# Performance work log

Measured on AMD Instinct MI355X. Metric: run time of the kernel, lower is better.

The kernel has to match this reference:

```python
import jax, jax.numpy as jnp
import numpy as np

NODELEN = 17949
N_NODES = 512
N_EDGES = 4096
H2 = 768
EMB = 128
IN_DIM = 2 * NODELEN


def _seg_mean(h, src, dst, n):
    # gather neighbor features and mean-reduce per destination node
    msg = h[src]                                   # [E, F]
    s = jax.ops.segment_sum(msg, dst, num_segments=n)
    deg = jax.ops.segment_sum(jnp.ones((src.shape[0],), h.dtype), dst, num_segments=n)
    return s / jnp.maximum(deg, 1.0)[:, None]


def setup_inputs() -> dict:
    key = jax.random.key(0)
    ks = jax.random.split(key, 12)
    s = 0.02
    return {
        "x": jax.random.normal(ks[0], (N_NODES, NODELEN), jnp.float32),
        "edge_src": jax.random.randint(ks[1], (N_EDGES,), 0, N_NODES),
        "edge_dst": jax.random.randint(ks[2], (N_EDGES,), 0, N_NODES),
        "W_e2": jax.random.normal(ks[3], (H2, IN_DIM), jnp.float32) * s,
        "b_e2": jnp.zeros((H2,), jnp.float32),
        "W_e3": jax.random.normal(ks[4], (EMB, H2), jnp.float32) * s,
        "b_e3": jnp.zeros((EMB,), jnp.float32),
        "W_d1": jax.random.normal(ks[5], (H2, EMB), jnp.float32) * s,
        "b_d1": jnp.zeros((H2,), jnp.float32),
        "W_d3": jax.random.normal(ks[6], (IN_DIM, H2), jnp.float32) * s,
        "b_d3": jnp.zeros((IN_DIM,), jnp.float32),
    }


def reference(x, edge_src, edge_dst, W_e2, b_e2, W_e3, b_e3, W_d1, b_d1, W_d3, b_d3):
    n = x.shape[0]
    # depth-2 recursive GraphSAGE mean aggregation; agg[0]=0 after each hop
    h1 = _seg_mean(x, edge_src, edge_dst, n).at[:, 0].set(0.0)
    h2 = _seg_mean(h1, edge_src, edge_dst, n).at[:, 0].set(0.0)
    emb = jnp.concatenate([x, h2], axis=1)           # [N, 2*NODELEN]
    emb = emb.at[:, 0].set(0.0).at[:, NODELEN].set(0.0)
    # AutoEncoder (eval mode: dropout is identity)
    h = jax.nn.relu(emb @ W_e2.T + b_e2)
    encoded = h @ W_e3.T + b_e3
    h = jax.nn.relu(encoded @ W_d1.T + b_d1)
    decoded = h @ W_d3.T + b_d3
    return encoded, decoded
```

## Files before the change

### kernel.cpp

```cpp
#include <hip/hip_runtime.h>
#include <hip/hip_bf16.h>

#define NODELEN 17949
#define NN 512
#define NE 4096
#define H2 768
#define EMB 128
#define IN_DIM (2 * NODELEN)
#define KP1 35904
#define KITERS1 561
#define SPLITS 24
#define KCHUNK1 24

#define BM 128
#define BN 128
#define BK 64
#define LDT (BK + 8)

typedef __bf16 bf16x8 __attribute__((ext_vector_type(8)));
typedef float f32x4 __attribute__((ext_vector_type(4)));


__global__ void k_zero_int(int* p, int n) {
    int i = blockIdx.x * 256 + threadIdx.x;
    if (i < n) p[i] = 0;
}

__global__ void k_zero_f4(float4* p, int n4) {
    int i = blockIdx.x * 256 + threadIdx.x;
    if (i < n4) p[i] = make_float4(0.f, 0.f, 0.f, 0.f);
}

__global__ void k_deg(const int* __restrict__ dst, int* __restrict__ cnt) {
    int e = blockIdx.x * 256 + threadIdx.x;
    if (e < NE) atomicAdd(&cnt[dst[e]], 1);
}

__global__ void k_invdeg(const int* __restrict__ cnt, float* __restrict__ invdeg) {
    int i = blockIdx.x * 256 + threadIdx.x;
    if (i < NN) {
        int c = cnt[i];
        invdeg[i] = 1.0f / (float)(c > 1 ? c : 1);
    }
}

__global__ void k_scatter(const int* __restrict__ src, const int* __restrict__ dst,
                          const float* __restrict__ invdeg, float* __restrict__ A) {
    int e = blockIdx.x * 256 + threadIdx.x;
    if (e < NE) {
        int d = dst[e];
        atomicAdd(&A[(size_t)d * NN + src[e]], invdeg[d]);
    }
}

__global__ void k_a2(const float* __restrict__ A, __bf16* __restrict__ A2b) {
    int i = blockIdx.x;
    int t = threadIdx.x;
    __shared__ float row[NN];
    row[t] = A[(size_t)i * NN + t];
    row[t + 256] = A[(size_t)i * NN + 256 + t];
    __syncthreads();
    float a0 = 0.f, a1 = 0.f;
    for (int s = 0; s < NN; ++s) {
        float a = row[s];
        if (a != 0.f) {
            a0 += a * A[(size_t)s * NN + t];
            a1 += a * A[(size_t)s * NN + 256 + t];
        }
    }
    A2b[(size_t)i * NN + t] = (__bf16)a0;
    A2b[(size_t)i * NN + 256 + t] = (__bf16)a1;
}

__global__ void k_xt(const float* __restrict__ x, __bf16* __restrict__ xT) {
    __shared__ float t[64][65];
    int f0 = blockIdx.x * 64, s0 = blockIdx.y * 64;
    int tx = threadIdx.x & 63, ty = threadIdx.x >> 6;
#pragma unroll
    for (int r = 0; r < 16; ++r) {
        int f = f0 + tx;
        t[ty * 16 + r][tx] = (f < NODELEN) ? x[(size_t)(s0 + ty * 16 + r) * NODELEN + f] : 0.f;
    }
    __syncthreads();
#pragma unroll
    for (int r = 0; r < 16; ++r) {
        int f = f0 + ty * 16 + r;
        if (f < NODELEN) xT[(size_t)f * NN + s0 + tx] = (__bf16)t[tx][ty * 16 + r];
    }
}

__global__ void k_embx(const float* __restrict__ x, __bf16* __restrict__ embb) {
    int c = blockIdx.x * 256 + threadIdx.x;
    int n = blockIdx.y;
    if (c < NODELEN) {
        float v = (c == 0) ? 0.f : x[(size_t)n * NODELEN + c];
        embb[(size_t)n * KP1 + c] = (__bf16)v;
    } else {
        int cc = c - NODELEN;
        if (cc < KP1 - IN_DIM) embb[(size_t)n * KP1 + IN_DIM + cc] = (__bf16)0.f;
    }
}

__global__ void k_cvt_we2(const float* __restrict__ W, __bf16* __restrict__ Wb) {
    const int C8 = KP1 / 8;
    int idx = blockIdx.x * 256 + threadIdx.x;
    if (idx >= H2 * C8) return;
    int r = idx / C8, c8 = (idx % C8) * 8;
    __align__(16) __bf16 o[8];
    if (c8 + 8 <= IN_DIM) {
        const float2* p = (const float2*)(W + (size_t)r * IN_DIM + c8);
#pragma unroll
        for (int j = 0; j < 4; ++j) {
            float2 f = p[j];
            o[2 * j] = (__bf16)f.x;
            o[2 * j + 1] = (__bf16)f.y;
        }
    } else {
#pragma unroll
        for (int j = 0; j < 8; ++j) {
            int c = c8 + j;
            o[j] = (c < IN_DIM) ? (__bf16)W[(size_t)r * IN_DIM + c] : (__bf16)0.f;
        }
    }
    *(uint4*)&Wb[(size_t)r * KP1 + c8] = *(uint4*)o;
}


template <int EPI, bool BF16B>
__global__ __launch_bounds__(256) void gemm_k(
        const __bf16* __restrict__ A, int lda,
        const void* __restrict__ Bv, int ldb,
        int Nvalid, int kIters, int kChunk,
        float* __restrict__ Cf, int ldc, const float* __restrict__ bias,
        __bf16* __restrict__ Cb) {
    __shared__ __align__(16) __bf16 As[BM][LDT];
    __shared__ __align__(16) __bf16 Bs[BN][LDT];

    const int tid = threadIdx.x;
    const int m0 = blockIdx.x * BM;
    const int n0 = blockIdx.y * BN;
    const int z = blockIdx.z;

    int it0 = z * kChunk;
    int it1 = it0 + kChunk;
    if (it1 > kIters) it1 = kIters;

    const int wave = tid >> 6;
    const int lane = tid & 63;
    const int wm = (wave & 1) * 64;
    const int wn = (wave >> 1) * 64;
    const int fl = lane & 15;
    const int fq = lane >> 4;

    const int srow = tid >> 1;
    const int spart = tid & 1;

    f32x4 acc[4][4] = {};

    const int bn = n0 + srow;
    const bool nok = bn < Nvalid;

    for (int it = it0; it < it1; ++it) {
        int k0 = it * BK;

        {
            const uint4* Ag = (const uint4*)(A + (size_t)(m0 + srow) * lda + k0 + spart * 32);
            uint4 av[4];
#pragma unroll
            for (int i = 0; i < 4; ++i) av[i] = Ag[i];
#pragma unroll
            for (int i = 0; i < 4; ++i)
                *(uint4*)&As[srow][spart * 32 + i * 8] = av[i];
        }
        if (BF16B) {
            uint4 bv[4];
            if (nok) {
                const uint4* Bg = (const uint4*)((const __bf16*)Bv + (size_t)bn * ldb + k0 + spart * 32);
#pragma unroll
                for (int i = 0; i < 4; ++i) bv[i] = Bg[i];
            } else {
#pragma unroll
                for (int i = 0; i < 4; ++i) bv[i] = make_uint4(0, 0, 0, 0);
            }
#pragma unroll
            for (int i = 0; i < 4; ++i)
                *(uint4*)&Bs[srow][spart * 32 + i * 8] = bv[i];
        } else {
            __align__(16) __bf16 bl[32];
            if (nok) {
                const float4* Bg = (const float4*)((const float*)Bv + (size_t)bn * ldb + k0 + spart * 32);
                float4 f[8];
#pragma unroll
                for (int j = 0; j < 8; ++j) f[j] = Bg[j];
#pragma unroll
                for (int j = 0; j < 8; ++j) {
                    bl[4 * j] = (__bf16)f[j].x;
                    bl[4 * j + 1] = (__bf16)f[j].y;
                    bl[4 * j + 2] = (__bf16)f[j].z;
                    bl[4 * j + 3] = (__bf16)f[j].w;
                }
            } else {
#pragma unroll
                for (int j = 0; j < 32; ++j) bl[j] = (__bf16)0.f;
            }
#pragma unroll
            for (int q = 0; q < 4; ++q)
                *(uint4*)&Bs[srow][spart * 32 + q * 8] = *(uint4*)&bl[q * 8];
        }
        __syncthreads();

#pragma unroll
        for (int ks = 0; ks < 2; ++ks) {
            int kk = ks * 32 + fq * 8;
            bf16x8 af[4], bf[4];
#pragma unroll
            for (int i = 0; i < 4; ++i)
                af[i] = *(const bf16x8*)&As[wm + i * 16 + fl][kk];
#pragma unroll
            for (int j = 0; j < 4; ++j)
                bf[j] = *(const bf16x8*)&Bs[wn + j * 16 + fl][kk];
#pragma unroll
            for (int i = 0; i < 4; ++i)
#pragma unroll
                for (int j = 0; j < 4; ++j)
                    acc[i][j] = __builtin_amdgcn_mfma_f32_16x16x32_bf16(
                        af[i], bf[j], acc[i][j], 0, 0, 0);
        }
        __syncthreads();
    }

#pragma unroll
    for (int i = 0; i < 4; ++i) {
#pragma unroll
        for (int j = 0; j < 4; ++j) {
#pragma unroll
            for (int r = 0; r < 4; ++r) {
                int m = m0 + wm + i * 16 + fq * 4 + r;
                int n = n0 + wn + j * 16 + fl;
                float v = acc[i][j][r];
                if (EPI == 0) {
                    Cf[((size_t)z * NN + m) * H2 + n] = v;
                } else if (EPI == 1) {
                    if (n < Nvalid) Cf[(size_t)m * ldc + n] = v + bias[n];
                } else {
                    if (n < Nvalid)
                        Cb[(size_t)m * KP1 + NODELEN + n] = (n == 0) ? (__bf16)0.f : (__bf16)v;
                }
            }
        }
    }
}

__global__ void k_reduce(const float* __restrict__ partials,
                         const float* __restrict__ bias, float* __restrict__ h) {
    int idx = blockIdx.x * 256 + threadIdx.x;
    if (idx >= NN * H2) return;
    float s = 0.f;
#pragma unroll
    for (int zz = 0; zz < SPLITS; ++zz) s += partials[(size_t)zz * NN * H2 + idx];
    s += bias[idx % H2];
    h[idx] = s > 0.f ? s : 0.f;
}

__global__ void k_enc(const float* __restrict__ h, const float* __restrict__ W,
                      const float* __restrict__ b, float* __restrict__ out) {
    int m = blockIdx.x, e = threadIdx.x;
    const float4* hr = (const float4*)(h + (size_t)m * H2);
    const float4* wr = (const float4*)(W + (size_t)e * H2);
    float s = 0.f;
#pragma unroll 4
    for (int i = 0; i < H2 / 4; ++i) {
        float4 a = hr[i];
        float4 w = wr[i];
        s += a.x * w.x + a.y * w.y + a.z * w.z + a.w * w.w;
    }
    out[(size_t)m * EMB + e] = s + b[e];
}

__global__ void k_dec1(const float* __restrict__ enc, const float* __restrict__ W,
                       const float* __restrict__ b, __bf16* __restrict__ hd) {
    int m = blockIdx.x;
    __shared__ float er[EMB];
    if (threadIdx.x < EMB) er[threadIdx.x] = enc[(size_t)m * EMB + threadIdx.x];
    __syncthreads();
    for (int j = threadIdx.x; j < H2; j += 256) {
        const float4* wr = (const float4*)(W + (size_t)j * EMB);
        float s = 0.f;
#pragma unroll
        for (int i = 0; i < EMB / 4; ++i) {
            float4 w = wr[i];
            s += w.x * er[4 * i] + w.y * er[4 * i + 1] + w.z * er[4 * i + 2] +
                 w.w * er[4 * i + 3];
        }
        float v = s + b[j];
        hd[(size_t)m * H2 + j] = (__bf16)(v > 0.f ? v : 0.f);
    }
}


extern "C" void kernel_launch(void* const* d_in, const int* in_sizes, int n_in,
                              void* d_out, int out_size, void* d_ws, size_t ws_size,
                              hipStream_t stream) {
    const float* x = (const float*)d_in[0];
    const int* esrc = (const int*)d_in[1];
    const int* edst = (const int*)d_in[2];
    const float* W_e2 = (const float*)d_in[3];
    const float* b_e2 = (const float*)d_in[4];
    const float* W_e3 = (const float*)d_in[5];
    const float* b_e3 = (const float*)d_in[6];
    const float* W_d1 = (const float*)d_in[7];
    const float* b_d1 = (const float*)d_in[8];
    const float* W_d3 = (const float*)d_in[9];
    const float* b_d3 = (const float*)d_in[10];
    float* out = (float*)d_out;

    char* w = (char*)d_ws;
    auto alloc = [&](size_t bytes) {
        char* p = w;
        w += (bytes + 255) & ~(size_t)255;
        return p;
    };
    __bf16* embb = (__bf16*)alloc((size_t)NN * KP1 * 2);
    __bf16* We2b = (__bf16*)alloc((size_t)H2 * KP1 * 2);
    char* uni = (char*)alloc((size_t)SPLITS * NN * H2 * 4);
    __bf16* xTb = (__bf16*)uni;
    float* Adj = (float*)(uni + (size_t)17952 * NN * 2);
    __bf16* A2b = (__bf16*)((char*)Adj + (size_t)NN * NN * 4);
    int* cnt = (int*)((char*)A2b + (size_t)NN * NN * 2);
    float* invdeg = (float*)((char*)cnt + 2048);
    float* partials = (float*)uni;
    float* h = (float*)alloc((size_t)NN * H2 * 4);
    __bf16* hd_b = (__bf16*)alloc((size_t)NN * H2 * 2);

    k_zero_int<<<2, 256, 0, stream>>>(cnt, NN);
    k_zero_f4<<<256, 256, 0, stream>>>((float4*)Adj, NN * NN / 4);
    k_deg<<<NE / 256, 256, 0, stream>>>(edst, cnt);
    k_invdeg<<<2, 256, 0, stream>>>(cnt, invdeg);
    k_scatter<<<NE / 256, 256, 0, stream>>>(esrc, edst, invdeg, Adj);
    k_a2<<<NN, 256, 0, stream>>>(Adj, A2b);

    dim3 gxt((NODELEN + 63) / 64, NN / 64);
    k_xt<<<gxt, 256, 0, stream>>>(x, xTb);
    dim3 gex((NODELEN + 255) / 256, NN);
    k_embx<<<gex, 256, 0, stream>>>(x, embb);

    dim3 gh2(NN / BM, (NODELEN + BN - 1) / BN, 1);
    gemm_k<2, true><<<gh2, 256, 0, stream>>>(
        A2b, NN, xTb, NN, NODELEN, NN / BK, NN / BK,
        (float*)nullptr, 0, (const float*)nullptr, embb);

    k_cvt_we2<<<(H2 * (KP1 / 8) + 255) / 256, 256, 0, stream>>>(W_e2, We2b);

    dim3 g1(NN / BM, H2 / BN, SPLITS);
    gemm_k<0, true><<<g1, 256, 0, stream>>>(
        embb, KP1, We2b, KP1, H2, KITERS1, KCHUNK1,
        partials, 0, (const float*)nullptr, (__bf16*)nullptr);

    k_reduce<<<(NN * H2) / 256, 256, 0, stream>>>(partials, b_e2, h);

    k_enc<<<NN, EMB, 0, stream>>>(h, W_e3, b_e3, out);

    k_dec1<<<NN, 256, 0, stream>>>(out, W_d1, b_d1, hd_b);

    dim3 g4(NN / BM, (IN_DIM + BN - 1) / BN, 1);
    gemm_k<1, false><<<g4, 256, 0, stream>>>(
        hd_b, H2, W_d3, H2, IN_DIM, H2 / BK, H2 / BK,
        out + (size_t)NN * EMB, IN_DIM, b_d3, (__bf16*)nullptr);
}
```

Baseline: 591.7 us.

## Reassociate GraphSAGE aggregation after the encoder GEMM and widen decoder GEMM tiles

The encoder's first layer is rewritten as x'·[W1;W2]^T followed by a small A²·Z2 propagation in fp32. This drops the large A²·x GEMM, the x transpose and the concatenated embedding buffer. The split-K GEMM now produces a 1536-wide output, the adjacency square stays in fp32, and a fused kernel applies the propagation, bias and ReLU. The decoder GEMM now uses blocks that cover all 512 rows, so each W_d3 tile is read and converted once. The costs are larger LDS use per block and simple per-element conversion kernels.

```diff
diff --git a/kernel.cpp b/kernel.cpp
--- a/kernel.cpp
+++ b/kernel.cpp
@@ -7,10 +7,11 @@
 #define H2 768
 #define EMB 128
 #define IN_DIM (2 * NODELEN)
-#define KP1 35904
-#define KITERS1 561
-#define SPLITS 24
-#define KCHUNK1 24
+#define KX 17984
+#define NKI 281
+#define NZ 1536
+#define SPLITS 16
+#define KCHUNK 18
 
 #define BM 128
 #define BN 128
@@ -53,7 +54,7 @@
     }
 }
 
-__global__ void k_a2(const float* __restrict__ A, __bf16* __restrict__ A2b) {
+__global__ void k_a2f(const float* __restrict__ A, float* __restrict__ A2) {
     int i = blockIdx.x;
     int t = threadIdx.x;
     __shared__ float row[NN];
@@ -68,71 +69,35 @@
             a1 += a * A[(size_t)s * NN + 256 + t];
         }
     }
-    A2b[(size_t)i * NN + t] = (__bf16)a0;
-    A2b[(size_t)i * NN + 256 + t] = (__bf16)a1;
-}
-
-__global__ void k_xt(const float* __restrict__ x, __bf16* __restrict__ xT) {
-    __shared__ float t[64][65];
-    int f0 = blockIdx.x * 64, s0 = blockIdx.y * 64;
-    int tx = threadIdx.x & 63, ty = threadIdx.x >> 6;
-#pragma unroll
-    for (int r = 0; r < 16; ++r) {
-        int f = f0 + tx;
-        t[ty * 16 + r][tx] = (f < NODELEN) ? x[(size_t)(s0 + ty * 16 + r) * NODELEN + f] : 0.f;
-    }
-    __syncthreads();
-#pragma unroll
-    for (int r = 0; r < 16; ++r) {
-        int f = f0 + ty * 16 + r;
-        if (f < NODELEN) xT[(size_t)f * NN + s0 + tx] = (__bf16)t[tx][ty * 16 + r];
-    }
-}
-
-__global__ void k_embx(const float* __restrict__ x, __bf16* __restrict__ embb) {
-    int c = blockIdx.x * 256 + threadIdx.x;
-    int n = blockIdx.y;
-    if (c < NODELEN) {
-        float v = (c == 0) ? 0.f : x[(size_t)n * NODELEN + c];
-        embb[(size_t)n * KP1 + c] = (__bf16)v;
-    } else {
-        int cc = c - NODELEN;
-        if (cc < KP1 - IN_DIM) embb[(size_t)n * KP1 + IN_DIM + cc] = (__bf16)0.f;
-    }
-}
-
-__global__ void k_cvt_we2(const float* __restrict__ W, __bf16* __restrict__ Wb) {
-    const int C8 = KP1 / 8;
-    int idx = blockIdx.x * 256 + threadIdx.x;
-    if (idx >= H2 * C8) return;
-    int r = idx / C8, c8 = (idx % C8) * 8;
-    __align__(16) __bf16 o[8];
-    if (c8 + 8 <= IN_DIM) {
-        const float2* p = (const float2*)(W + (size_t)r * IN_DIM + c8);
-#pragma unroll
-        for (int j = 0; j < 4; ++j) {
-            float2 f = p[j];
-            o[2 * j] = (__bf16)f.x;
-            o[2 * j + 1] = (__bf16)f.y;
-        }
-    } else {
-#pragma unroll
-        for (int j = 0; j < 8; ++j) {
-            int c = c8 + j;
-            o[j] = (c < IN_DIM) ? (__bf16)W[(size_t)r * IN_DIM + c] : (__bf16)0.f;
-        }
-    }
-    *(uint4*)&Wb[(size_t)r * KP1 + c8] = *(uint4*)o;
-}
-
-
-template <int EPI, bool BF16B>
-__global__ __launch_bounds__(256) void gemm_k(
-        const __bf16* __restrict__ A, int lda,
-        const void* __restrict__ Bv, int ldb,
-        int Nvalid, int kIters, int kChunk,
-        float* __restrict__ Cf, int ldc, const float* __restrict__ bias,
-        __bf16* __restrict__ Cb) {
+    A2[(size_t)i * NN + t] = a0;
+    A2[(size_t)i * NN + 256 + t] = a1;
+}
+
+__global__ void k_xb(const float* __restrict__ x, __bf16* __restrict__ xb) {
+    size_t idx = (size_t)blockIdx.x * 256 + threadIdx.x;
+    if (idx >= (size_t)NN * KX) return;
+    int n = (int)(idx / KX), k = (int)(idx % KX);
+    float v = (k == 0 || k >= NODELEN) ? 0.f : x[(size_t)n * NODELEN + k];
+    xb[idx] = (__bf16)v;
+}
+
+__global__ void k_wb(const float* __restrict__ W, __bf16* __restrict__ Wb) {
+    size_t idx = (size_t)blockIdx.x * 256 + threadIdx.x;
+    if (idx >= (size_t)NZ * KX) return;
+    int n = (int)(idx / KX), k = (int)(idx % KX);
+    float v = 0.f;
+    if (k < NODELEN) {
+        int r = n, c = k;
+        if (n >= H2) { r = n - H2; c = k + NODELEN; }
+        v = W[(size_t)r * IN_DIM + c];
+    }
+    Wb[idx] = (__bf16)v;
+}
+
+
+__global__ __launch_bounds__(256) void gemm_splitk(
+        const __bf16* __restrict__ A, const __bf16* __restrict__ B,
+        float* __restrict__ partials) {
     __shared__ __align__(16) __bf16 As[BM][LDT];
     __shared__ __align__(16) __bf16 Bs[BN][LDT];
 
@@ -141,9 +106,9 @@
     const int n0 = blockIdx.y * BN;
     const int z = blockIdx.z;
 
-    int it0 = z * kChunk;
-    int it1 = it0 + kChunk;
-    if (it1 > kIters) it1 = kIters;
+    int it0 = z * KCHUNK;
+    int it1 = it0 + KCHUNK;
+    if (it1 > NKI) it1 = NKI;
 
     const int wave = tid >> 6;
     const int lane = tid & 63;
@@ -157,14 +122,10 @@
 
     f32x4 acc[4][4] = {};
 
-    const int bn = n0 + srow;
-    const bool nok = bn < Nvalid;
-
     for (int it = it0; it < it1; ++it) {
         int k0 = it * BK;
-
         {
-            const uint4* Ag = (const uint4*)(A + (size_t)(m0 + srow) * lda + k0 + spart * 32);
+            const uint4* Ag = (const uint4*)(A + (size_t)(m0 + srow) * KX + k0 + spart * 32);
             uint4 av[4];
 #pragma unroll
             for (int i = 0; i < 4; ++i) av[i] = Ag[i];
@@ -172,40 +133,14 @@
             for (int i = 0; i < 4; ++i)
                 *(uint4*)&As[srow][spart * 32 + i * 8] = av[i];
         }
-        if (BF16B) {
+        {
+            const uint4* Bg = (const uint4*)(B + (size_t)(n0 + srow) * KX + k0 + spart * 32);
             uint4 bv[4];
-            if (nok) {
-                const uint4* Bg = (const uint4*)((const __bf16*)Bv + (size_t)bn * ldb + k0 + spart * 32);
-#pragma unroll
-                for (int i = 0; i < 4; ++i) bv[i] = Bg[i];
-            } else {
-#pragma unroll
-                for (int i = 0; i < 4; ++i) bv[i] = make_uint4(0, 0, 0, 0);
-            }
+#pragma unroll
+            for (int i = 0; i < 4; ++i) bv[i] = Bg[i];
 #pragma unroll
             for (int i = 0; i < 4; ++i)
                 *(uint4*)&Bs[srow][spart * 32 + i * 8] = bv[i];
-        } else {
-            __align__(16) __bf16 bl[32];
-            if (nok) {
-                const float4* Bg = (const float4*)((const float*)Bv + (size_t)bn * ldb + k0 + spart * 32);
-                float4 f[8];
-#pragma unroll
-                for (int j = 0; j < 8; ++j) f[j] = Bg[j];
-#pragma unroll
-                for (int j = 0; j < 8; ++j) {
-                    bl[4 * j] = (__bf16)f[j].x;
-                    bl[4 * j + 1] = (__bf16)f[j].y;
-                    bl[4 * j + 2] = (__bf16)f[j].z;
-                    bl[4 * j + 3] = (__bf16)f[j].w;
-                }
-            } else {
-#pragma unroll
-                for (int j = 0; j < 32; ++j) bl[j] = (__bf16)0.f;
-            }
-#pragma unroll
-            for (int q = 0; q < 4; ++q)
-                *(uint4*)&Bs[srow][spart * 32 + q * 8] = *(uint4*)&bl[q * 8];
         }
         __syncthreads();
 
@@ -230,36 +165,52 @@
     }
 
 #pragma unroll
-    for (int i = 0; i < 4; ++i) {
-#pragma unroll
-        for (int j = 0; j < 4; ++j) {
+    for (int i = 0; i < 4; ++i)
+#pragma unroll
+        for (int j = 0; j < 4; ++j)
 #pragma unroll
             for (int r = 0; r < 4; ++r) {
                 int m = m0 + wm + i * 16 + fq * 4 + r;
                 int n = n0 + wn + j * 16 + fl;
-                float v = acc[i][j][r];
-                if (EPI == 0) {
-                    Cf[((size_t)z * NN + m) * H2 + n] = v;
-                } else if (EPI == 1) {
-                    if (n < Nvalid) Cf[(size_t)m * ldc + n] = v + bias[n];
-                } else {
-                    if (n < Nvalid)
-                        Cb[(size_t)m * KP1 + NODELEN + n] = (n == 0) ? (__bf16)0.f : (__bf16)v;
-                }
+                partials[((size_t)z * NN + m) * NZ + n] = acc[i][j][r];
             }
-        }
-    }
-}
-
-__global__ void k_reduce(const float* __restrict__ partials,
-                         const float* __restrict__ bias, float* __restrict__ h) {
+}
+
+__global__ void k_reduceZ(const float* __restrict__ partials, float* __restrict__ Z) {
     int idx = blockIdx.x * 256 + threadIdx.x;
-    if (idx >= NN * H2) return;
+    if (idx >= NN * NZ) return;
     float s = 0.f;
 #pragma unroll
-    for (int zz = 0; zz < SPLITS; ++zz) s += partials[(size_t)zz * NN * H2 + idx];
-    s += bias[idx % H2];
-    h[idx] = s > 0.f ? s : 0.f;
+    for (int zz = 0; zz < SPLITS; ++zz) s += partials[(size_t)zz * NN * NZ + idx];
+    Z[idx] = s;
+}
+
+__global__ void k_fuse(const float* __restrict__ A2, const float* __restrict__ Z,
+                       const float* __restrict__ b, float* __restrict__ h) {
+    int i = blockIdx.x;
+    int t = threadIdx.x;
+    __shared__ float row[NN];
+    row[t] = A2[(size_t)i * NN + t];
+    row[t + 256] = A2[(size_t)i * NN + 256 + t];
+    __syncthreads();
+    float s0 = 0.f, s1 = 0.f, s2 = 0.f;
+    for (int s = 0; s < NN; ++s) {
+        float a = row[s];
+        if (a != 0.f) {
+            const float* zr = Z + (size_t)s * NZ + H2;
+            s0 += a * zr[t];
+            s1 += a * zr[t + 256];
+            s2 += a * zr[t + 512];
+        }
+    }
+    const float* zl = Z + (size_t)i * NZ;
+    float v0 = zl[t] + s0 + b[t];
+    float v1 = zl[t + 256] + s1 + b[t + 256];
+    float v2 = zl[t + 512] + s2 + b[t + 512];
+    float* hr = h + (size_t)i * H2;
+    hr[t] = v0 > 0.f ? v0 : 0.f;
+    hr[t + 256] = v1 > 0.f ? v1 : 0.f;
+    hr[t + 512] = v2 > 0.f ? v2 : 0.f;
 }
 
 __global__ void k_enc(const float* __restrict__ h, const float* __restrict__ W,
@@ -295,6 +246,93 @@
         float v = s + b[j];
         hd[(size_t)m * H2 + j] = (__bf16)(v > 0.f ? v : 0.f);
     }
+}
+
+
+#define WBN 64
+#define WBK 64
+#define ALD 68
+#define BLD 72
+
+__global__ __launch_bounds__(256, 2) void gemm_wide(
+        const __bf16* __restrict__ A, const float* __restrict__ B,
+        const float* __restrict__ bias, float* __restrict__ C) {
+    __shared__ __align__(16) __bf16 As[NN * ALD];
+    __shared__ __align__(16) __bf16 Bs[WBN * BLD];
+
+    const int tid = threadIdx.x;
+    const int n0 = blockIdx.x * WBN;
+    const int wave = tid >> 6, lane = tid & 63;
+    const int fl = lane & 15, fq = lane >> 4;
+    const int wm = wave * 128;
+
+    const int brow = tid >> 2;
+    const int bcol = (tid & 3) * 16;
+    const int gn = n0 + brow;
+    const bool bok = gn < IN_DIM;
+
+    f32x4 acc[8][4] = {};
+
+    for (int it = 0; it < H2 / WBK; ++it) {
+        int k0 = it * WBK;
+#pragma unroll
+        for (int q = 0; q < 16; ++q) {
+            int g = tid + 256 * q;
+            int r = g >> 3, c8 = (g & 7) * 8;
+            uint4 v = *(const uint4*)(A + (size_t)r * H2 + k0 + c8);
+            *(uint4*)&As[r * ALD + c8] = v;
+        }
+        {
+            __align__(16) __bf16 bl[16];
+            if (bok) {
+                const float4* bg = (const float4*)(B + (size_t)gn * H2 + k0 + bcol);
+#pragma unroll
+                for (int j = 0; j < 4; ++j) {
+                    float4 f = bg[j];
+                    bl[4 * j] = (__bf16)f.x;
+                    bl[4 * j + 1] = (__bf16)f.y;
+                    bl[4 * j + 2] = (__bf16)f.z;
+                    bl[4 * j + 3] = (__bf16)f.w;
+                }
+            } else {
+#pragma unroll
+                for (int j = 0; j < 16; ++j) bl[j] = (__bf16)0.f;
+            }
+            *(uint4*)&Bs[brow * BLD + bcol] = *(uint4*)&bl[0];
+            *(uint4*)&Bs[brow * BLD + bcol + 8] = *(uint4*)&bl[8];
+        }
+        __syncthreads();
+
+#pragma unroll
+        for (int ks = 0; ks < 2; ++ks) {
+            int kk = ks * 32 + fq * 8;
+            bf16x8 bfr[4];
+#pragma unroll
+            for (int j = 0; j < 4; ++j)
+                bfr[j] = *(const bf16x8*)&Bs[(j * 16 + fl) * BLD + kk];
+#pragma unroll
+            for (int i = 0; i < 8; ++i) {
+                bf16x8 afr = *(const bf16x8*)&As[(wm + i * 16 + fl) * ALD + kk];
+#pragma unroll
+                for (int j = 0; j < 4; ++j)
+                    acc[i][j] = __builtin_amdgcn_mfma_f32_16x16x32_bf16(
+                        afr, bfr[j], acc[i][j], 0, 0, 0);
+            }
+        }
+        __syncthreads();
+    }
+
+#pragma unroll
+    for (int i = 0; i < 8; ++i)
+#pragma unroll
+        for (int j = 0; j < 4; ++j)
+#pragma unroll
+            for (int r = 0; r < 4; ++r) {
+                int m = wm + i * 16 + fq * 4 + r;
+                int n = n0 + j * 16 + fl;
+                if (n < IN_DIM)
+                    C[(size_t)m * IN_DIM + n] = acc[i][j][r] + bias[n];
+            }
 }
 
 
@@ -320,15 +358,14 @@
         w += (bytes + 255) & ~(size_t)255;
         return p;
     };
-    __bf16* embb = (__bf16*)alloc((size_t)NN * KP1 * 2);
-    __bf16* We2b = (__bf16*)alloc((size_t)H2 * KP1 * 2);
-    char* uni = (char*)alloc((size_t)SPLITS * NN * H2 * 4);
-    __bf16* xTb = (__bf16*)uni;
-    float* Adj = (float*)(uni + (size_t)17952 * NN * 2);
-    __bf16* A2b = (__bf16*)((char*)Adj + (size_t)NN * NN * 4);
-    int* cnt = (int*)((char*)A2b + (size_t)NN * NN * 2);
-    float* invdeg = (float*)((char*)cnt + 2048);
-    float* partials = (float*)uni;
+    __bf16* xb = (__bf16*)alloc((size_t)NN * KX * 2);
+    __bf16* Wb = (__bf16*)alloc((size_t)NZ * KX * 2);
+    float* partials = (float*)alloc((size_t)SPLITS * NN * NZ * 4);
+    float* Z = (float*)alloc((size_t)NN * NZ * 4);
+    float* Adj = (float*)alloc((size_t)NN * NN * 4);
+    float* A2f = (float*)alloc((size_t)NN * NN * 4);
+    int* cnt = (int*)alloc(NN * 4);
+    float* invdeg = (float*)alloc(NN * 4);
     float* h = (float*)alloc((size_t)NN * H2 * 4);
     __bf16* hd_b = (__bf16*)alloc((size_t)NN * H2 * 2);
 
@@ -337,33 +374,21 @@
     k_deg<<<NE / 256, 256, 0, stream>>>(edst, cnt);
     k_invdeg<<<2, 256, 0, stream>>>(cnt, invdeg);
     k_scatter<<<NE / 256, 256, 0, stream>>>(esrc, edst, invdeg, Adj);
-    k_a2<<<NN, 256, 0, stream>>>(Adj, A2b);
-
-    dim3 gxt((NODELEN + 63) / 64, NN / 64);
-    k_xt<<<gxt, 256, 0, stream>>>(x, xTb);
-    dim3 gex((NODELEN + 255) / 256, NN);
-    k_embx<<<gex, 256, 0, stream>>>(x, embb);
-
-    dim3 gh2(NN / BM, (NODELEN + BN - 1) / BN, 1);
-    gemm_k<2, true><<<gh2, 256, 0, stream>>>(
-        A2b, NN, xTb, NN, NODELEN, NN / BK, NN / BK,
-        (float*)nullptr, 0, (const float*)nullptr, embb);
-
-    k_cvt_we2<<<(H2 * (KP1 / 8) + 255) / 256, 256, 0, stream>>>(W_e2, We2b);
-
-    dim3 g1(NN / BM, H2 / BN, SPLITS);
-    gemm_k<0, true><<<g1, 256, 0, stream>>>(
-        embb, KP1, We2b, KP1, H2, KITERS1, KCHUNK1,
-        partials, 0, (const float*)nullptr, (__bf16*)nullptr);
-
-    k_reduce<<<(NN * H2) / 256, 256, 0, stream>>>(partials, b_e2, h);
+    k_a2f<<<NN, 256, 0, stream>>>(Adj, A2f);
+
+    k_xb<<<(int)(((size_t)NN * KX + 255) / 256), 256, 0, stream>>>(x, xb);
+    k_wb<<<(int)(((size_t)NZ * KX + 255) / 256), 256, 0, stream>>>(W_e2, Wb);
+
+    dim3 gz(NN / BM, NZ / BN, SPLITS);
+    gemm_splitk<<<gz, 256, 0, stream>>>(xb, Wb, partials);
+    k_reduceZ<<<(NN * NZ) / 256, 256, 0, stream>>>(partials, Z);
+
+    k_fuse<<<NN, 256, 0, stream>>>(A2f, Z, b_e2, h);
 
     k_enc<<<NN, EMB, 0, stream>>>(h, W_e3, b_e3, out);
 
     k_dec1<<<NN, 256, 0, stream>>>(out, W_d1, b_d1, hd_b);
 
-    dim3 g4(NN / BM, (IN_DIM + BN - 1) / BN, 1);
-    gemm_k<1, false><<<g4, 256, 0, stream>>>(
-        hd_b, H2, W_d3, H2, IN_DIM, H2 / BK, H2 / BK,
-        out + (size_t)NN * EMB, IN_DIM, b_d3, (__bf16*)nullptr);
-}
+    gemm_wide<<<(IN_DIM + WBN - 1) / WBN, 256, 0, stream>>>(
+        hd_b, W_d3, b_d3, out + (size_t)NN * EMB);
+}
```

Result: slower. 673.0 us (+13.7%).
